# Performance work log

Hardware: AMD Instinct MI355X
Metric: run time of the kernel (lower is better)

Reference implementation:

```python
import jax, jax.numpy as jnp
import numpy as np

# FitzHugh-Nagumo / Model_FN constants (from __init__)
A_ = 0.7; B_ = 0.8; EPI = 0.2; TAU = 0.1; I_ = 1.0; K_ = 1.0; W_ = 1.0
STRENGTH = 1.0; UMAX = 10.0; D_SM = 0.1; EPS_REG = 1e-3
DIM = 1024; N = 4096


def smooth_relu(x, d=D_SM):
    r = jnp.maximum(x, 0.0)
    sq = (2.0 * d * r ** 3 - r ** 4) / (2.0 * d ** 3)
    return jnp.where(r < d, sq, x - d / 2.0)


def temp_L(t, P):
    # vectorized version of Model_FN.temp_L: sum_i eig_i * v_i^T v_i, i=1..dim-1
    dim = P.shape[0]
    i = jnp.arange(1, dim)
    s = 2.0 * K_ * jnp.sin(W_ * t)                      # [1]
    thresh = int(dim + 1) / 2 - 1                       # float threshold, as in source
    eig = jnp.where(i <= thresh, 1.0 + s, 1.0 - s)      # [dim-1]
    V = P[1:]                                           # [dim-1, dim]
    return V.T @ (eig[:, None] * V)                     # [dim, dim]


def control_net(x, W1, b1, W2, b2, W3, b3):
    # ControlNet.forward: u = MLP(x); bound(u * x)
    h1 = jnp.tanh(x @ W1.T + b1)
    h2 = jnp.tanh(h1 @ W2.T + b2)
    u = h2 @ W3.T + b3
    ux = u * x
    ux = jnp.where(ux < UMAX, ux, 0.0)
    return jnp.where(-UMAX < ux, ux, 0.0)


def icnn_fn(x, ws, bs, us):
    # ICNN.icnn_fn: x [N, d_in] -> z [1, N]
    xt = x.T                                            # [d_in, N]
    z = smooth_relu(ws[0] @ xt + bs[0])
    for i in range(len(us)):
        z = smooth_relu(ws[i + 1] @ xt + bs[i + 1] + jax.nn.softplus(us[i]) @ z)
    return z


def setup_inputs() -> dict:
    key = jax.random.key(0)
    ks = jax.random.split(key, 20)
    d_in = 2 * DIM
    inp = {
        'state': jax.random.normal(ks[0], (N, d_in), jnp.float32),
        't': jax.random.uniform(ks[1], (1,), jnp.float32) * 10.0,
        'P': jax.random.normal(ks[2], (DIM, DIM), jnp.float32) / np.sqrt(DIM),
        # ControlNet weights (SpectralNorm wrapper undefined in source -> plain Linear)
        'W1': jax.random.normal(ks[3], (512, d_in), jnp.float32) / np.sqrt(d_in),
        'b1': jax.random.normal(ks[4], (512,), jnp.float32) * 0.01,
        'W2': jax.random.normal(ks[5], (512, 512), jnp.float32) / np.sqrt(512),
        'b2': jax.random.normal(ks[6], (512,), jnp.float32) * 0.01,
        'W3': jax.random.normal(ks[7], (d_in, 512), jnp.float32) / np.sqrt(512),
        'b3': jax.random.normal(ks[8], (d_in,), jnp.float32) * 0.01,
        # ICNN parameters, layer_sizes=[64, 64, 1]
        'icW0': jax.random.normal(ks[9], (64, d_in), jnp.float32) / np.sqrt(d_in),
        'icb0': jax.random.normal(ks[10], (64, 1), jnp.float32) * 0.01,
        'icW1': jax.random.normal(ks[11], (64, d_in), jnp.float32) / np.sqrt(d_in),
        'icb1': jax.random.normal(ks[12], (64, 1), jnp.float32) * 0.01,
        'icW2': jax.random.normal(ks[13], (1, d_in), jnp.float32) / np.sqrt(d_in),
        'icb2': jax.random.normal(ks[14], (1, 1), jnp.float32) * 0.01,
        'icU0': jax.random.normal(ks[15], (64, 64), jnp.float32) / np.sqrt(64),
        'icU1': jax.random.normal(ks[16], (1, 64), jnp.float32) / np.sqrt(64),
    }
    return inp


def reference(state, t, P, W1, b1, W2, b2, W3, b3,
              icW0, icb0, icW1, icb1, icW2, icb2, icU0, icU1):
    dim = state.shape[1] // 2
    u, v = state[:, :dim], state[:, dim:]

    # FN drift with time-varying Laplacian coupling (Model_FN.FN)
    Lm = temp_L(t, P)                                   # [dim, dim]
    Hu = jax.nn.sigmoid(u / TAU)                        # H(u)
    du = u - u ** 3 / 3.0 - v + I_ + STRENGTH * (Hu @ Lm.T)
    dv = EPI * (u + A_ - B_ * v)
    dx = jnp.concatenate([du, dv], axis=1)              # [N, 2*dim]

    # ControlNet on synchronization deviations (Model_FN.FN_g state transform)
    st = jnp.concatenate([u - u[:, :1], v - v[:, :1]], axis=1)
    ctrl = control_net(st, W1, b1, W2, b2, W3, b3)
    dx_total = dx + ctrl

    # ICNN Lyapunov value (ICNN.forward)
    ws, bs, us = [icW0, icW1, icW2], [icb0, icb1, icb2], [icU0, icU1]
    z = icnn_fn(state, ws, bs, us)                      # [1, N]
    z0 = icnn_fn(jnp.zeros_like(state), ws, bs, us)     # [1, N]
    regular = EPS_REG * jnp.sum(state ** 2, axis=1, keepdims=True)
    V = smooth_relu(z - z0).T + regular                 # [N, 1]

    return jnp.concatenate([dx_total, V], axis=1)       # [N, 2*dim + 1]
```

## Files before the change

### kernel.cpp

```cpp
#include <hip/hip_runtime.h>
#include <hip/hip_fp8.h>
#include <cstdint>
#include <cstddef>

using short8 = __attribute__((ext_vector_type(8))) short;
using f32x4  = __attribute__((ext_vector_type(4))) float;
using bfraw  = unsigned short;

__device__ __forceinline__ bfraw f2b(float f){
  unsigned int u = __builtin_bit_cast(unsigned int, f);
  u += 0x7FFFu + ((u >> 16) & 1u);
  return (bfraw)(u >> 16);
}
__device__ __forceinline__ float b2f(bfraw h){
  unsigned int u = ((unsigned int)h) << 16;
  return __builtin_bit_cast(float, u);
}
__device__ __forceinline__ unsigned char f2f8(float f){
  __hip_fp8_e4m3 t(f);
  return (unsigned char)t.__x;
}
__device__ __forceinline__ float srelu(float x){
  float r = fmaxf(x, 0.0f);
  if (r < 0.1f){ float r2 = r * r; return (0.2f * r2 * r - r2 * r2) * 500.0f; }
  return x - 0.05f;
}
__device__ __forceinline__ float softplusf(float x){
  return (x > 15.0f) ? x : log1pf(expf(x));
}
__device__ __forceinline__ void gload16(const void* g, void* s){
  __builtin_amdgcn_global_load_lds((const __attribute__((address_space(1))) void*)g,
                                   (__attribute__((address_space(3))) void*)s, 16, 0, 0);
}
template<int N> __device__ __forceinline__ void wait_vm(){
  if constexpr (N == 0)      asm volatile("s_waitcnt vmcnt(0)" ::: "memory");
  else if constexpr (N == 2) asm volatile("s_waitcnt vmcnt(2)" ::: "memory");
  else if constexpr (N == 3) asm volatile("s_waitcnt vmcnt(3)" ::: "memory");
  else                       asm volatile("s_waitcnt vmcnt(4)" ::: "memory");
}
__device__ __forceinline__ void block_barrier(){
  __builtin_amdgcn_s_barrier();
  asm volatile("" ::: "memory");
}

constexpr size_t OFF_STATEB = 0;
constexpr size_t OFF_STATE8 = 16777216;
constexpr size_t OFF_HUB    = 25165824;
constexpr size_t OFF_PT     = 29360128;
constexpr size_t OFF_PTEIG  = 31457280;
constexpr size_t OFF_LM8    = 33554432;
constexpr size_t OFF_W1F8   = 34603008;
constexpr size_t OFF_ICWB   = 35651584;
constexpr size_t OFF_W28    = 36175872;
constexpr size_t OFF_W38    = 36438016;
constexpr size_t OFF_H18    = 37486592;
constexpr size_t OFF_H28    = 39583744;
constexpr size_t OFF_Z1F    = 41680896;
constexpr size_t OFF_Z2PRE  = 42729472;
constexpr size_t OFF_SPU0   = 43778048;
constexpr size_t OFF_SPU1   = 43794432;
constexpr size_t OFF_Z0     = 43794688;
constexpr size_t OFF_SU1    = 43794944;
constexpr size_t OFF_SV1    = 43796992;
constexpr size_t OFF_U0     = 43799040;
constexpr size_t OFF_V0     = 43815424;

__global__ __launch_bounds__(256) void prep_all(const float* __restrict__ W1,
    const float* __restrict__ icW0, const float* __restrict__ icW1,
    const float* __restrict__ W2, const float* __restrict__ W3,
    const float* __restrict__ P, const float* __restrict__ tptr,
    const float* __restrict__ icU0, const float* __restrict__ icU1,
    const float* __restrict__ icb0, const float* __restrict__ icb1, const float* __restrict__ icb2,
    const float* __restrict__ state,
    unsigned char* __restrict__ w1f8, bfraw* __restrict__ icwb,
    unsigned char* __restrict__ w28, unsigned char* __restrict__ w3f8,
    bfraw* __restrict__ PT, bfraw* __restrict__ PTeig,
    float* __restrict__ su1, float* __restrict__ sv1,
    float* __restrict__ spU0, float* __restrict__ spU1, float* __restrict__ z0out,
    bfraw* __restrict__ stateb, unsigned char* __restrict__ state8, unsigned char* __restrict__ hub8,
    float* __restrict__ u0a, float* __restrict__ v0a){
  __shared__ float smem[4288];
  const int b = blockIdx.x;
  const int t = threadIdx.x;
  if (b < 2560){
    const int i4 = (b * 256 + t) * 4;
    if (i4 >= 1048576 && i4 < 1310720){
      const float* src = (i4 < 1179648) ? icW0 : icW1;
      const int off = (i4 < 1179648) ? (i4 - 1048576) : (i4 - 1179648);
      const int dsto = i4 - 1048576;
      float4 v = *reinterpret_cast<const float4*>(src + off);
      ushort4 o;
      o.x = f2b(v.x); o.y = f2b(v.y); o.z = f2b(v.z); o.w = f2b(v.w);
      *reinterpret_cast<ushort4*>(icwb + dsto) = o;
    } else {
      const float* src; unsigned char* dst; int off;
      if (i4 < 1048576)      { src = W1; dst = w1f8; off = i4; }
      else if (i4 < 1572864) { src = W2; dst = w28;  off = i4 - 1310720; }
      else                   { src = W3; dst = w3f8; off = i4 - 1572864; }
      float4 v = *reinterpret_cast<const float4*>(src + off);
      uchar4 o;
      o.x = f2f8(v.x); o.y = f2f8(v.y); o.z = f2f8(v.z); o.w = f2f8(v.w);
      *reinterpret_cast<uchar4*>(dst + off) = o;
    }
  } else if (b < 3584){
    float (*tile)[33] = (float(*)[33])smem;
    const int idx = b - 2560;
    const int bi = idx >> 5, bj = idx & 31;
    const int tx = t & 31, ty = t >> 5;
    #pragma unroll
    for (int r = 0; r < 4; ++r){
      const int k = bj * 32 + ty + r * 8;
      const int i = bi * 32 + tx;
      tile[ty + r * 8][tx] = P[(size_t)k * 1024 + i];
    }
    __syncthreads();
    const float s = 2.0f * sinf(tptr[0]);
    #pragma unroll
    for (int r = 0; r < 4; ++r){
      const int i = bi * 32 + ty + r * 8;
      const int k = bj * 32 + tx;
      const float p = tile[tx][ty + r * 8];
      const float e = (k == 0) ? 0.0f : ((k <= 511) ? (1.0f + s) : (1.0f - s));
      PT[(size_t)i * 1024 + k] = f2b(p);
      PTeig[(size_t)i * 1024 + k] = f2b(e * p);
    }
  } else if (b < 4096){
    const int n = b - 3584;
    float a = 0.0f, bb = 0.0f;
    for (int j = t; j < 1024; j += 256) a += W1[(size_t)n * 2048 + j];
    for (int j = t; j < 1024; j += 256) bb += W1[(size_t)n * 2048 + 1024 + j];
    #pragma unroll
    for (int o = 32; o > 0; o >>= 1){ a += __shfl_down(a, o, 64); bb += __shfl_down(bb, o, 64); }
    if ((t & 63) == 0){ smem[t >> 6] = a; smem[4 + (t >> 6)] = bb; }
    __syncthreads();
    if (t == 0){
      su1[n] = smem[0] + smem[1] + smem[2] + smem[3];
      sv1[n] = smem[4] + smem[5] + smem[6] + smem[7];
    }
  } else if (b == 4096){
    float* sp  = smem;
    float* sp1 = smem + 4096;
    float* a0  = smem + 4160;
    float* a1  = smem + 4224;
    #pragma unroll
    for (int i = 0; i < 16; ++i){
      const int idx = i * 256 + t;
      const float v = softplusf(icU0[idx]);
      sp[idx] = v;
      spU0[idx] = v;
    }
    if (t < 64){
      const float v1 = softplusf(icU1[t]);
      sp1[t] = v1;
      spU1[t] = v1;
      a0[t] = srelu(icb0[t]);
    }
    __syncthreads();
    {
      const int n = t >> 2, q = t & 3;
      float sAcc = 0.0f;
      #pragma unroll
      for (int j = 0; j < 16; ++j) sAcc += sp[n * 64 + q * 16 + j] * a0[q * 16 + j];
      sAcc += __shfl_down(sAcc, 2, 64);
      sAcc += __shfl_down(sAcc, 1, 64);
      if (q == 0) a1[n] = srelu(sAcc + icb1[n]);
    }
    __syncthreads();
    if (t < 64){
      float v = sp1[t] * a1[t];
      #pragma unroll
      for (int o = 32; o > 0; o >>= 1) v += __shfl_down(v, o, 64);
      if (t == 0) z0out[0] = srelu(v + icb2[0]);
    }
  } else {
    const int row = b - 4097;
    const float* srow = state + (size_t)row * 2048;
    float4 u4 = *reinterpret_cast<const float4*>(srow + t * 4);
    float4 v4 = *reinterpret_cast<const float4*>(srow + 1024 + t * 4);
    float us[4] = {u4.x, u4.y, u4.z, u4.w};
    float vs[4] = {v4.x, v4.y, v4.z, v4.w};
    uchar4 h8, s8u, s8v;
    unsigned char* hp = reinterpret_cast<unsigned char*>(&h8);
    unsigned char* su = reinterpret_cast<unsigned char*>(&s8u);
    unsigned char* sv = reinterpret_cast<unsigned char*>(&s8v);
    #pragma unroll
    for (int i = 0; i < 4; ++i){
      const int j = t * 4 + i;
      const float u = us[i], v = vs[i];
      stateb[(size_t)row * 2048 + j] = f2b(u);
      stateb[(size_t)row * 2048 + 1024 + j] = f2b(v);
      su[i] = f2f8(u);
      sv[i] = f2f8(v);
      hp[i] = f2f8(1.0f / (1.0f + expf(-10.0f * u)));
    }
    *reinterpret_cast<uchar4*>(state8 + (size_t)row * 2048 + t * 4) = s8u;
    *reinterpret_cast<uchar4*>(state8 + (size_t)row * 2048 + 1024 + t * 4) = s8v;
    *reinterpret_cast<uchar4*>(hub8 + (size_t)row * 1024 + t * 4) = h8;
    if (t == 0){ u0a[row] = srow[0]; v0a[row] = srow[1024]; }
  }
}

__global__ __launch_bounds__(256) void v2_kernel(const bfraw* __restrict__ stateb, const float* __restrict__ icW2,
    const float* __restrict__ z1f, const float* __restrict__ z2pre,
    const float* __restrict__ spU0, const float* __restrict__ spU1,
    const float* __restrict__ z0p, const float* __restrict__ icb2, float* __restrict__ out){
  const int row = blockIdx.x;
  const int t = threadIdx.x;
  __shared__ float z1s[64];
  __shared__ float s1[4], s2[4];
  if (t < 64) z1s[t] = z1f[(size_t)row * 64 + t];
  short8 xv = reinterpret_cast<const short8*>(stateb + (size_t)row * 2048)[t];
  float4 w0 = reinterpret_cast<const float4*>(icW2)[t * 2];
  float4 w1 = reinterpret_cast<const float4*>(icW2)[t * 2 + 1];
  float wv[8] = {w0.x, w0.y, w0.z, w0.w, w1.x, w1.y, w1.z, w1.w};
  float d = 0.0f, ss = 0.0f;
  #pragma unroll
  for (int e = 0; e < 8; ++e){
    const float x = b2f((bfraw)xv[e]);
    d  = fmaf(wv[e], x, d);
    ss = fmaf(x, x, ss);
  }
  #pragma unroll
  for (int o = 32; o > 0; o >>= 1){ d += __shfl_down(d, o, 64); ss += __shfl_down(ss, o, 64); }
  if ((t & 63) == 0){ s1[t >> 6] = d; s2[t >> 6] = ss; }
  __syncthreads();
  if (t < 64){
    float acc2 = z2pre[(size_t)row * 64 + t];
    #pragma unroll 8
    for (int j = 0; j < 64; ++j) acc2 += spU0[t * 64 + j] * z1s[j];
    float dd = spU1[t] * srelu(acc2);
    #pragma unroll
    for (int o = 32; o > 0; o >>= 1) dd += __shfl_down(dd, o, 64);
    if (t == 0){
      const float D = dd + s1[0] + s1[1] + s1[2] + s1[3];
      const float S = s2[0] + s2[1] + s2[2] + s2[3];
      const float z3 = srelu(D + icb2[0]);
      out[(size_t)row * 2049 + 2048] = srelu(z3 - z0p[0]) + 0.001f * S;
    }
  }
}

__global__ __launch_bounds__(512)
void gemm_mid(const bfraw* __restrict__ pteig, const bfraw* __restrict__ pt,
              unsigned char* __restrict__ lm8,
              const bfraw* __restrict__ stateb, const bfraw* __restrict__ icwb,
              const float* __restrict__ icb0, const float* __restrict__ icb1,
              float* __restrict__ z1f, float* __restrict__ z2pre)
{
  __shared__ bfraw lA[3][64 * 64];
  __shared__ bfraw lB[3][64 * 64];
  const int blk = blockIdx.x;
  const bool isLm = (blk < 256);
  const bfraw* A; const bfraw* B; int K, bm, bn;
  if (isLm){ A = pteig; B = pt; K = 1024; bm = blk >> 4; bn = blk & 15; }
  else     { const int i = blk - 256; A = stateb; B = icwb; K = 2048; bm = i >> 1; bn = i & 1; }
  const int tid = threadIdx.x;
  const int w  = tid >> 6;
  const int l  = tid & 63;
  const int wr = w >> 2;
  const int wc = w & 3;
  const int lr = l & 15;
  const int q  = l >> 4;

  f32x4 acc[2] = {};
  const int nt = K >> 6;

  auto stage = [&](int buf, int k0){
    const int r = tid >> 3;
    const int kc = (tid & 7) ^ (r & 7);
    gload16(A + (size_t)(bm * 64 + r) * K + k0 + kc * 8, &lA[buf][(size_t)(w * 64) * 8]);
    gload16(B + (size_t)(bn * 64 + r) * K + k0 + kc * 8, &lB[buf][(size_t)(w * 64) * 8]);
  };

  stage(0, 0);
  stage(1, 64);
  for (int t = 0; t < nt; ++t){
    const int cur = t % 3;
    if (t == nt - 1) wait_vm<0>(); else wait_vm<2>();
    block_barrier();
    short8 aF[2][2], bF[2];
    #pragma unroll
    for (int kh = 0; kh < 2; ++kh){
      const int kch = (kh * 4 + q) ^ (lr & 7);
      #pragma unroll
      for (int m = 0; m < 2; ++m){
        const int R = wr * 32 + m * 16 + lr;
        aF[kh][m] = *reinterpret_cast<const short8*>(&lA[cur][(size_t)R * 64 + kch * 8]);
      }
      const int R = wc * 16 + lr;
      bF[kh] = *reinterpret_cast<const short8*>(&lB[cur][(size_t)R * 64 + kch * 8]);
    }
    if (t + 2 < nt) stage((t + 2) % 3, (t + 2) * 64);
    #pragma unroll
    for (int kh = 0; kh < 2; ++kh)
      #pragma unroll
      for (int m = 0; m < 2; ++m)
        acc[m] = __builtin_amdgcn_mfma_f32_16x16x32_bf16(aF[kh][m], bF[kh], acc[m], 0, 0, 0);
  }

  #pragma unroll
  for (int m = 0; m < 2; ++m){
    #pragma unroll
    for (int r = 0; r < 4; ++r){
      const int row = bm * 64 + wr * 32 + m * 16 + q * 4 + r;
      const int c64 = wc * 16 + lr;
      const float v = acc[m][r];
      if (isLm){
        lm8[(size_t)row * 1024 + bn * 64 + c64] = f2f8(v);
      } else if (bn == 0){
        z1f[(size_t)row * 64 + c64] = srelu(v + icb0[c64]);
      } else {
        z2pre[(size_t)row * 64 + c64] = v + icb1[c64];
      }
    }
  }
}

template<int EPI, int TM, int TN>
__global__ __launch_bounds__(512)
void gemm_nt8(const unsigned char* __restrict__ A, const unsigned char* __restrict__ B,
              int N, int K,
              const float* __restrict__ bias, unsigned char* __restrict__ outf8,
              const float* __restrict__ u0a, const float* __restrict__ v0a,
              const float* __restrict__ su1, const float* __restrict__ sv1)
{
  constexpr int MF = TM / 32;
  constexpr int NF = TN / 64;
  constexpr int LPB = TM / 64 + TN / 64;
  __shared__ unsigned char lA[3][TM * 128];
  __shared__ unsigned char lB[3][TN * 128];
  const int tid = threadIdx.x;
  const int w  = tid >> 6;
  const int l  = tid & 63;
  const int wr = w >> 2;
  const int wc = w & 3;
  const int bm = blockIdx.x;
  const int bn = blockIdx.y;
  const int lr = l & 15;
  const int q  = l >> 4;

  f32x4 acc[MF][NF] = {};
  const int nt = K >> 7;

  auto stage = [&](int buf, int k0){
    #pragma unroll
    for (int j = 0; j < TM / 64; ++j){
      const int c = j * 512 + tid;
      const int r = c >> 3;
      const int kc = (c & 7) ^ (r & 7);
      gload16(A + (size_t)(bm * TM + r) * K + k0 + kc * 16, &lA[buf][(size_t)(j * 512 + w * 64) * 16]);
    }
    #pragma unroll
    for (int j = 0; j < TN / 64; ++j){
      const int c = j * 512 + tid;
      const int r = c >> 3;
      const int kc = (c & 7) ^ (r & 7);
      gload16(B + (size_t)(bn * TN + r) * K + k0 + kc * 16, &lB[buf][(size_t)(j * 512 + w * 64) * 16]);
    }
  };

  stage(0, 0);
  stage(1, 128);
  for (int t = 0; t < nt; ++t){
    const int cur = t % 3;
    if (t == nt - 1) wait_vm<0>(); else wait_vm<LPB>();
    block_barrier();
    long long aF[4][MF], bF[4][NF];
    #pragma unroll
    for (int kh = 0; kh < 4; ++kh){
      const int ko = kh * 32 + q * 8;
      const int ch = (ko >> 4) ^ (lr & 7);
      const int bo = ko & 15;
      #pragma unroll
      for (int m = 0; m < MF; ++m){
        const int R = wr * (TM / 2) + m * 16 + lr;
        aF[kh][m] = *reinterpret_cast<const long long*>(&lA[cur][(size_t)R * 128 + ch * 16 + bo]);
      }
      #pragma unroll
      for (int n = 0; n < NF; ++n){
        const int R = wc * (TN / 4) + n * 16 + lr;
        bF[kh][n] = *reinterpret_cast<const long long*>(&lB[cur][(size_t)R * 128 + ch * 16 + bo]);
      }
    }
    if (t + 2 < nt) stage((t + 2) % 3, (t + 2) * 128);
    #pragma unroll
    for (int kh = 0; kh < 4; ++kh){
      #pragma unroll
      for (int m = 0; m < MF; ++m){
        #pragma unroll
        for (int n = 0; n < NF; ++n){
          acc[m][n] = __builtin_amdgcn_mfma_f32_16x16x32_fp8_fp8(aF[kh][m], bF[kh][n], acc[m][n], 0, 0, 0);
        }
      }
    }
  }

  #pragma unroll
  for (int m = 0; m < MF; ++m){
    #pragma unroll
    for (int n = 0; n < NF; ++n){
      #pragma unroll
      for (int r = 0; r < 4; ++r){
        const int row = bm * TM + wr * (TM / 2) + m * 16 + q * 4 + r;
        const int col = bn * TN + wc * (TN / 4) + n * 16 + lr;
        const float v = acc[m][n][r];
        if constexpr (EPI == 1){
          const float h = v - u0a[row] * su1[col] - v0a[row] * sv1[col] + bias[col];
          outf8[(size_t)row * N + col] = f2f8(tanhf(h));
        } else {
          outf8[(size_t)row * N + col] = f2f8(tanhf(v + bias[col]));
        }
      }
    }
  }
}

__global__ __launch_bounds__(512, 4)
void gemm_out(const unsigned char* __restrict__ hub8, const unsigned char* __restrict__ lm8,
              const unsigned char* __restrict__ h2b8, const unsigned char* __restrict__ w3f8,
              const bfraw* __restrict__ stateb, const float* __restrict__ b3,
              const float* __restrict__ u0a, const float* __restrict__ v0a,
              float* __restrict__ out)
{
  __shared__ unsigned char lA[128 * 128];
  __shared__ unsigned char lBlo[64 * 128];
  __shared__ unsigned char lBhi[64 * 128];
  const int tid = threadIdx.x;
  const int w  = tid >> 6;
  const int l  = tid & 63;
  const int wr = w >> 2;
  const int wc = w & 3;
  const int bm = blockIdx.x;
  const int bn = blockIdx.y;
  const int lr = l & 15;
  const int q  = l >> 4;

  const unsigned char* Au  = h2b8 + (size_t)(bm * 128) * 512;
  const unsigned char* Bwl = w3f8 + (size_t)(bn * 64) * 512;
  const unsigned char* Bwh = w3f8 + (size_t)(1024 + bn * 64) * 512;
  const unsigned char* Ah  = hub8 + (size_t)(bm * 128) * 1024;
  const unsigned char* Bl  = lm8  + (size_t)(bn * 64) * 1024;

  f32x4 acc2[4] = {};
  f32x4 acc3[4] = {};

  for (int t = 0; t < 4; ++t){
    const int k0 = t * 128;
    #pragma unroll
    for (int j = 0; j < 2; ++j){
      const int c = j * 512 + tid;
      const int r = c >> 3;
      const int kc = (c & 7) ^ (r & 7);
      gload16(Au + (size_t)r * 512 + k0 + kc * 16, &lA[(size_t)(j * 512 + w * 64) * 16]);
    }
    {
      const int r = tid >> 3;
      const int kc = (tid & 7) ^ (r & 7);
      gload16(Bwl + (size_t)r * 512 + k0 + kc * 16, &lBlo[(size_t)(w * 64) * 16]);
      gload16(Bwh + (size_t)r * 512 + k0 + kc * 16, &lBhi[(size_t)(w * 64) * 16]);
    }
    __syncthreads();
    #pragma unroll
    for (int kh = 0; kh < 4; ++kh){
      const int ko = kh * 32 + q * 8;
      const int ch = (ko >> 4) ^ (lr & 7);
      const int bo = ko & 15;
      long long aF[4], bL, bH;
      #pragma unroll
      for (int m = 0; m < 4; ++m){
        const int R = wr * 64 + m * 16 + lr;
        aF[m] = *reinterpret_cast<const long long*>(&lA[(size_t)R * 128 + ch * 16 + bo]);
      }
      const int Rb = wc * 16 + lr;
      bL = *reinterpret_cast<const long long*>(&lBlo[(size_t)Rb * 128 + ch * 16 + bo]);
      bH = *reinterpret_cast<const long long*>(&lBhi[(size_t)Rb * 128 + ch * 16 + bo]);
      #pragma unroll
      for (int m = 0; m < 4; ++m){
        acc2[m] = __builtin_amdgcn_mfma_f32_16x16x32_fp8_fp8(aF[m], bL, acc2[m], 0, 0, 0);
        acc3[m] = __builtin_amdgcn_mfma_f32_16x16x32_fp8_fp8(aF[m], bH, acc3[m], 0, 0, 0);
      }
    }
    __syncthreads();
  }

  #pragma unroll
  for (int m = 0; m < 4; ++m){
    #pragma unroll
    for (int r = 0; r < 4; ++r){
      const int row = bm * 128 + wr * 64 + m * 16 + q * 4 + r;
      const int c   = bn * 64 + wc * 16 + lr;
      const float un = acc3[m][r] + b3[1024 + c];
      const float u  = b2f(stateb[(size_t)row * 2048 + c]);
      const float vv = b2f(stateb[(size_t)row * 2048 + 1024 + c]);
      const float x  = vv - v0a[row];
      const float ux = un * x;
      const float cl = (ux < 10.0f && -10.0f < ux) ? ux : 0.0f;
      out[(size_t)row * 2049 + 1024 + c] = 0.2f * (u + 0.7f - 0.8f * vv) + cl;
    }
  }

  f32x4 acc1[4] = {};
  for (int t = 0; t < 8; ++t){
    const int k0 = t * 128;
    #pragma unroll
    for (int j = 0; j < 2; ++j){
      const int c = j * 512 + tid;
      const int r = c >> 3;
      const int kc = (c & 7) ^ (r & 7);
      gload16(Ah + (size_t)r * 1024 + k0 + kc * 16, &lA[(size_t)(j * 512 + w * 64) * 16]);
    }
    {
      const int r = tid >> 3;
      const int kc = (tid & 7) ^ (r & 7);
      gload16(Bl + (size_t)r * 1024 + k0 + kc * 16, &lBlo[(size_t)(w * 64) * 16]);
    }
    __syncthreads();
    #pragma unroll
    for (int kh = 0; kh < 4; ++kh){
      const int ko = kh * 32 + q * 8;
      const int ch = (ko >> 4) ^ (lr & 7);
      const int bo = ko & 15;
      long long aF[4], bL;
      #pragma unroll
      for (int m = 0; m < 4; ++m){
        const int R = wr * 64 + m * 16 + lr;
        aF[m] = *reinterpret_cast<const long long*>(&lA[(size_t)R * 128 + ch * 16 + bo]);
      }
      const int Rb = wc * 16 + lr;
      bL = *reinterpret_cast<const long long*>(&lBlo[(size_t)Rb * 128 + ch * 16 + bo]);
      #pragma unroll
      for (int m = 0; m < 4; ++m){
        acc1[m] = __builtin_amdgcn_mfma_f32_16x16x32_fp8_fp8(aF[m], bL, acc1[m], 0, 0, 0);
      }
    }
    __syncthreads();
  }

  #pragma unroll
  for (int m = 0; m < 4; ++m){
    #pragma unroll
    for (int r = 0; r < 4; ++r){
      const int row = bm * 128 + wr * 64 + m * 16 + q * 4 + r;
      const int c   = bn * 64 + wc * 16 + lr;
      const float un = acc2[m][r] + b3[c];
      const float u  = b2f(stateb[(size_t)row * 2048 + c]);
      const float vv = b2f(stateb[(size_t)row * 2048 + 1024 + c]);
      const float x  = u - u0a[row];
      const float ux = un * x;
      const float cl = (ux < 10.0f && -10.0f < ux) ? ux : 0.0f;
      out[(size_t)row * 2049 + c] = acc1[m][r] + u - u * u * u * (1.0f / 3.0f) - vv + 1.0f + cl;
    }
  }
}

extern "C" void kernel_launch(void* const* d_in, const int* in_sizes, int n_in,
                              void* d_out, int out_size, void* d_ws, size_t ws_size,
                              hipStream_t stream){
  (void)in_sizes; (void)n_in; (void)out_size; (void)ws_size;
  const float* state = (const float*)d_in[0];
  const float* tp    = (const float*)d_in[1];
  const float* P     = (const float*)d_in[2];
  const float* W1    = (const float*)d_in[3];
  const float* b1    = (const float*)d_in[4];
  const float* W2    = (const float*)d_in[5];
  const float* b2    = (const float*)d_in[6];
  const float* W3    = (const float*)d_in[7];
  const float* b3    = (const float*)d_in[8];
  const float* icW0  = (const float*)d_in[9];
  const float* icb0  = (const float*)d_in[10];
  const float* icW1  = (const float*)d_in[11];
  const float* icb1  = (const float*)d_in[12];
  const float* icW2  = (const float*)d_in[13];
  const float* icb2  = (const float*)d_in[14];
  const float* icU0  = (const float*)d_in[15];
  const float* icU1  = (const float*)d_in[16];
  float* out = (float*)d_out;
  char* ws = (char*)d_ws;

  bfraw* stateb = (bfraw*)(ws + OFF_STATEB);
  unsigned char* state8 = (unsigned char*)(ws + OFF_STATE8);
  unsigned char* hub8   = (unsigned char*)(ws + OFF_HUB);
  bfraw* pt     = (bfraw*)(ws + OFF_PT);
  bfraw* pteig  = (bfraw*)(ws + OFF_PTEIG);
  unsigned char* lm8  = (unsigned char*)(ws + OFF_LM8);
  unsigned char* w1f8 = (unsigned char*)(ws + OFF_W1F8);
  bfraw* icwb   = (bfraw*)(ws + OFF_ICWB);
  unsigned char* w28  = (unsigned char*)(ws + OFF_W28);
  unsigned char* w3f8 = (unsigned char*)(ws + OFF_W38);
  unsigned char* h18  = (unsigned char*)(ws + OFF_H18);
  unsigned char* h28  = (unsigned char*)(ws + OFF_H28);
  float* z1f    = (float*)(ws + OFF_Z1F);
  float* z2pre  = (float*)(ws + OFF_Z2PRE);
  float* spU0   = (float*)(ws + OFF_SPU0);
  float* spU1   = (float*)(ws + OFF_SPU1);
  float* z0     = (float*)(ws + OFF_Z0);
  float* su1    = (float*)(ws + OFF_SU1);
  float* sv1    = (float*)(ws + OFF_SV1);
  float* u0a    = (float*)(ws + OFF_U0);
  float* v0a    = (float*)(ws + OFF_V0);

  prep_all<<<dim3(8193), 256, 0, stream>>>(W1, icW0, icW1, W2, W3, P, tp,
      icU0, icU1, icb0, icb1, icb2, state,
      w1f8, icwb, w28, w3f8, pt, pteig, su1, sv1, spU0, spU1, z0,
      stateb, state8, hub8, u0a, v0a);

  gemm_mid<<<dim3(384), 512, 0, stream>>>(pteig, pt, lm8, stateb, icwb, icb0, icb1, z1f, z2pre);
  gemm_nt8<1, 64, 128><<<dim3(64, 4), 512, 0, stream>>>(state8, w1f8, 512, 2048,
      b1, h18, u0a, v0a, su1, sv1);
  gemm_nt8<2, 64, 128><<<dim3(64, 4), 512, 0, stream>>>(h18, w28, 512, 512,
      b2, h28, nullptr, nullptr, nullptr, nullptr);
  gemm_out<<<dim3(32, 16), 512, 0, stream>>>(hub8, lm8, h28, w3f8, stateb, b3, u0a, v0a, out);

  v2_kernel<<<dim3(4096), 256, 0, stream>>>(stateb, icW2, z1f, z2pre, spU0, spU1, z0, icb2, out);
}
```

Before: 101.5 us.

## Merge independent kernels via block-index dispatch to cut launch count

Folds the first ControlNet layer GEMM into the Laplacian/ICNN mid GEMM launch as extra blocks, and folds the per-row ICNN value kernel into the output GEMM launch as trailing blocks using a shared raw LDS buffer. This takes the pipeline from six launches to four and lets independent work share one grid, reducing launch gaps and tail idle time. The value blocks now use 512 threads with 4 elements each. The costs are larger LDS allocations for the merged blocks, which can lower occupancy, and mixed block types inside one grid.

New measurement: 95.37 us, median of 2. 1.06x faster.

```diff
diff --git a/kernel.cpp b/kernel.cpp
--- a/kernel.cpp
+++ b/kernel.cpp
@@ -200,135 +200,164 @@
   }
 }
 
-__global__ __launch_bounds__(256) void v2_kernel(const bfraw* __restrict__ stateb, const float* __restrict__ icW2,
-    const float* __restrict__ z1f, const float* __restrict__ z2pre,
-    const float* __restrict__ spU0, const float* __restrict__ spU1,
-    const float* __restrict__ z0p, const float* __restrict__ icb2, float* __restrict__ out){
-  const int row = blockIdx.x;
-  const int t = threadIdx.x;
-  __shared__ float z1s[64];
-  __shared__ float s1[4], s2[4];
-  if (t < 64) z1s[t] = z1f[(size_t)row * 64 + t];
-  short8 xv = reinterpret_cast<const short8*>(stateb + (size_t)row * 2048)[t];
-  float4 w0 = reinterpret_cast<const float4*>(icW2)[t * 2];
-  float4 w1 = reinterpret_cast<const float4*>(icW2)[t * 2 + 1];
-  float wv[8] = {w0.x, w0.y, w0.z, w0.w, w1.x, w1.y, w1.z, w1.w};
-  float d = 0.0f, ss = 0.0f;
-  #pragma unroll
-  for (int e = 0; e < 8; ++e){
-    const float x = b2f((bfraw)xv[e]);
-    d  = fmaf(wv[e], x, d);
-    ss = fmaf(x, x, ss);
-  }
-  #pragma unroll
-  for (int o = 32; o > 0; o >>= 1){ d += __shfl_down(d, o, 64); ss += __shfl_down(ss, o, 64); }
-  if ((t & 63) == 0){ s1[t >> 6] = d; s2[t >> 6] = ss; }
-  __syncthreads();
-  if (t < 64){
-    float acc2 = z2pre[(size_t)row * 64 + t];
-    #pragma unroll 8
-    for (int j = 0; j < 64; ++j) acc2 += spU0[t * 64 + j] * z1s[j];
-    float dd = spU1[t] * srelu(acc2);
-    #pragma unroll
-    for (int o = 32; o > 0; o >>= 1) dd += __shfl_down(dd, o, 64);
-    if (t == 0){
-      const float D = dd + s1[0] + s1[1] + s1[2] + s1[3];
-      const float S = s2[0] + s2[1] + s2[2] + s2[3];
-      const float z3 = srelu(D + icb2[0]);
-      out[(size_t)row * 2049 + 2048] = srelu(z3 - z0p[0]) + 0.001f * S;
-    }
-  }
-}
-
 __global__ __launch_bounds__(512)
-void gemm_mid(const bfraw* __restrict__ pteig, const bfraw* __restrict__ pt,
-              unsigned char* __restrict__ lm8,
-              const bfraw* __restrict__ stateb, const bfraw* __restrict__ icwb,
-              const float* __restrict__ icb0, const float* __restrict__ icb1,
-              float* __restrict__ z1f, float* __restrict__ z2pre)
+void gemm_midh1(const bfraw* __restrict__ pteig, const bfraw* __restrict__ pt,
+                unsigned char* __restrict__ lm8,
+                const bfraw* __restrict__ stateb, const bfraw* __restrict__ icwb,
+                const float* __restrict__ icb0, const float* __restrict__ icb1,
+                float* __restrict__ z1f, float* __restrict__ z2pre,
+                const unsigned char* __restrict__ state8, const unsigned char* __restrict__ w1f8,
+                const float* __restrict__ b1, unsigned char* __restrict__ h18,
+                const float* __restrict__ u0a, const float* __restrict__ v0a,
+                const float* __restrict__ su1, const float* __restrict__ sv1)
 {
-  __shared__ bfraw lA[3][64 * 64];
-  __shared__ bfraw lB[3][64 * 64];
+  __shared__ char ldsRaw[73728];
   const int blk = blockIdx.x;
-  const bool isLm = (blk < 256);
-  const bfraw* A; const bfraw* B; int K, bm, bn;
-  if (isLm){ A = pteig; B = pt; K = 1024; bm = blk >> 4; bn = blk & 15; }
-  else     { const int i = blk - 256; A = stateb; B = icwb; K = 2048; bm = i >> 1; bn = i & 1; }
   const int tid = threadIdx.x;
   const int w  = tid >> 6;
   const int l  = tid & 63;
-  const int wr = w >> 2;
-  const int wc = w & 3;
   const int lr = l & 15;
   const int q  = l >> 4;
 
-  f32x4 acc[2] = {};
-  const int nt = K >> 6;
-
-  auto stage = [&](int buf, int k0){
-    const int r = tid >> 3;
-    const int kc = (tid & 7) ^ (r & 7);
-    gload16(A + (size_t)(bm * 64 + r) * K + k0 + kc * 8, &lA[buf][(size_t)(w * 64) * 8]);
-    gload16(B + (size_t)(bn * 64 + r) * K + k0 + kc * 8, &lB[buf][(size_t)(w * 64) * 8]);
-  };
-
-  stage(0, 0);
-  stage(1, 64);
-  for (int t = 0; t < nt; ++t){
-    const int cur = t % 3;
-    if (t == nt - 1) wait_vm<0>(); else wait_vm<2>();
-    block_barrier();
-    short8 aF[2][2], bF[2];
-    #pragma unroll
-    for (int kh = 0; kh < 2; ++kh){
-      const int kch = (kh * 4 + q) ^ (lr & 7);
-      #pragma unroll
-      for (int m = 0; m < 2; ++m){
-        const int R = wr * 32 + m * 16 + lr;
-        aF[kh][m] = *reinterpret_cast<const short8*>(&lA[cur][(size_t)R * 64 + kch * 8]);
-      }
-      const int R = wc * 16 + lr;
-      bF[kh] = *reinterpret_cast<const short8*>(&lB[cur][(size_t)R * 64 + kch * 8]);
-    }
-    if (t + 2 < nt) stage((t + 2) % 3, (t + 2) * 64);
-    #pragma unroll
-    for (int kh = 0; kh < 2; ++kh)
-      #pragma unroll
-      for (int m = 0; m < 2; ++m)
-        acc[m] = __builtin_amdgcn_mfma_f32_16x16x32_bf16(aF[kh][m], bF[kh], acc[m], 0, 0, 0);
-  }
-
-  #pragma unroll
-  for (int m = 0; m < 2; ++m){
-    #pragma unroll
-    for (int r = 0; r < 4; ++r){
-      const int row = bm * 64 + wr * 32 + m * 16 + q * 4 + r;
-      const int c64 = wc * 16 + lr;
-      const float v = acc[m][r];
-      if (isLm){
-        lm8[(size_t)row * 1024 + bn * 64 + c64] = f2f8(v);
-      } else if (bn == 0){
-        z1f[(size_t)row * 64 + c64] = srelu(v + icb0[c64]);
-      } else {
-        z2pre[(size_t)row * 64 + c64] = v + icb1[c64];
-      }
-    }
-  }
-}
-
-template<int EPI, int TM, int TN>
+  if (blk < 384){
+    bfraw* lA = (bfraw*)ldsRaw;
+    bfraw* lB = (bfraw*)(ldsRaw + 24576);
+    const bool isLm = (blk < 256);
+    const bfraw* A; const bfraw* B; int K, bm, bn;
+    if (isLm){ A = pteig; B = pt; K = 1024; bm = blk >> 4; bn = blk & 15; }
+    else     { const int i = blk - 256; A = stateb; B = icwb; K = 2048; bm = i >> 1; bn = i & 1; }
+    const int wr = w >> 2;
+    const int wc = w & 3;
+    f32x4 acc[2] = {};
+    const int nt = K >> 6;
+    auto stage = [&](int buf, int k0){
+      const int r = tid >> 3;
+      const int kc = (tid & 7) ^ (r & 7);
+      gload16(A + (size_t)(bm * 64 + r) * K + k0 + kc * 8, &lA[(size_t)buf * 4096 + (size_t)(w * 64) * 8]);
+      gload16(B + (size_t)(bn * 64 + r) * K + k0 + kc * 8, &lB[(size_t)buf * 4096 + (size_t)(w * 64) * 8]);
+    };
+    stage(0, 0);
+    stage(1, 64);
+    for (int t = 0; t < nt; ++t){
+      const int cur = t % 3;
+      if (t == nt - 1) wait_vm<0>(); else wait_vm<2>();
+      block_barrier();
+      short8 aF[2][2], bF[2];
+      #pragma unroll
+      for (int kh = 0; kh < 2; ++kh){
+        const int kch = (kh * 4 + q) ^ (lr & 7);
+        #pragma unroll
+        for (int m = 0; m < 2; ++m){
+          const int R = wr * 32 + m * 16 + lr;
+          aF[kh][m] = *reinterpret_cast<const short8*>(&lA[(size_t)cur * 4096 + (size_t)R * 64 + kch * 8]);
+        }
+        const int R = wc * 16 + lr;
+        bF[kh] = *reinterpret_cast<const short8*>(&lB[(size_t)cur * 4096 + (size_t)R * 64 + kch * 8]);
+      }
+      if (t + 2 < nt) stage((t + 2) % 3, (t + 2) * 64);
+      #pragma unroll
+      for (int kh = 0; kh < 2; ++kh)
+        #pragma unroll
+        for (int m = 0; m < 2; ++m)
+          acc[m] = __builtin_amdgcn_mfma_f32_16x16x32_bf16(aF[kh][m], bF[kh], acc[m], 0, 0, 0);
+    }
+    #pragma unroll
+    for (int m = 0; m < 2; ++m){
+      #pragma unroll
+      for (int r = 0; r < 4; ++r){
+        const int row = bm * 64 + (w >> 2) * 32 + m * 16 + q * 4 + r;
+        const int c64 = (w & 3) * 16 + lr;
+        const float v = acc[m][r];
+        if (isLm){
+          lm8[(size_t)row * 1024 + bn * 64 + c64] = f2f8(v);
+        } else if (bn == 0){
+          z1f[(size_t)row * 64 + c64] = srelu(v + icb0[c64]);
+        } else {
+          z2pre[(size_t)row * 64 + c64] = v + icb1[c64];
+        }
+      }
+    }
+  } else {
+    unsigned char* lA = (unsigned char*)ldsRaw;
+    unsigned char* lB = (unsigned char*)(ldsRaw + 24576);
+    const int i = blk - 384;
+    const int bm = i >> 2;
+    const int bn = i & 3;
+    const int wr = w >> 2;
+    const int wc = w & 3;
+    constexpr int K = 2048;
+    f32x4 acc[2][2] = {};
+    const int nt = K >> 7;
+    auto stage = [&](int buf, int k0){
+      {
+        const int c = tid;
+        const int r = c >> 3;
+        const int kc = (c & 7) ^ (r & 7);
+        gload16(state8 + (size_t)(bm * 64 + r) * K + k0 + kc * 16, &lA[(size_t)buf * 8192 + (size_t)(w * 64) * 16]);
+      }
+      #pragma unroll
+      for (int j = 0; j < 2; ++j){
+        const int c = j * 512 + tid;
+        const int r = c >> 3;
+        const int kc = (c & 7) ^ (r & 7);
+        gload16(w1f8 + (size_t)(bn * 128 + r) * K + k0 + kc * 16, &lB[(size_t)buf * 16384 + (size_t)(j * 512 + w * 64) * 16]);
+      }
+    };
+    stage(0, 0);
+    stage(1, 128);
+    for (int t = 0; t < nt; ++t){
+      const int cur = t % 3;
+      if (t == nt - 1) wait_vm<0>(); else wait_vm<3>();
+      block_barrier();
+      long long aF[4][2], bF[4][2];
+      #pragma unroll
+      for (int kh = 0; kh < 4; ++kh){
+        const int ko = kh * 32 + q * 8;
+        const int ch = (ko >> 4) ^ (lr & 7);
+        const int bo = ko & 15;
+        #pragma unroll
+        for (int m = 0; m < 2; ++m){
+          const int R = wr * 32 + m * 16 + lr;
+          aF[kh][m] = *reinterpret_cast<const long long*>(&lA[(size_t)cur * 8192 + (size_t)R * 128 + ch * 16 + bo]);
+        }
+        #pragma unroll
+        for (int n = 0; n < 2; ++n){
+          const int R = wc * 32 + n * 16 + lr;
+          bF[kh][n] = *reinterpret_cast<const long long*>(&lB[(size_t)cur * 16384 + (size_t)R * 128 + ch * 16 + bo]);
+        }
+      }
+      if (t + 2 < nt) stage((t + 2) % 3, (t + 2) * 128);
+      #pragma unroll
+      for (int kh = 0; kh < 4; ++kh)
+        #pragma unroll
+        for (int m = 0; m < 2; ++m)
+          #pragma unroll
+          for (int n = 0; n < 2; ++n)
+            acc[m][n] = __builtin_amdgcn_mfma_f32_16x16x32_fp8_fp8(aF[kh][m], bF[kh][n], acc[m][n], 0, 0, 0);
+    }
+    #pragma unroll
+    for (int m = 0; m < 2; ++m){
+      #pragma unroll
+      for (int n = 0; n < 2; ++n){
+        #pragma unroll
+        for (int r = 0; r < 4; ++r){
+          const int row = bm * 64 + wr * 32 + m * 16 + q * 4 + r;
+          const int col = bn * 128 + wc * 32 + n * 16 + lr;
+          const float h = acc[m][n][r] - u0a[row] * su1[col] - v0a[row] * sv1[col] + b1[col];
+          h18[(size_t)row * 512 + col] = f2f8(tanhf(h));
+        }
+      }
+    }
+  }
+}
+
 __global__ __launch_bounds__(512)
-void gemm_nt8(const unsigned char* __restrict__ A, const unsigned char* __restrict__ B,
-              int N, int K,
-              const float* __restrict__ bias, unsigned char* __restrict__ outf8,
-              const float* __restrict__ u0a, const float* __restrict__ v0a,
-              const float* __restrict__ su1, const float* __restrict__ sv1)
+void gemm_h2(const unsigned char* __restrict__ A, const unsigned char* __restrict__ B,
+             const float* __restrict__ bias, unsigned char* __restrict__ outf8)
 {
-  constexpr int MF = TM / 32;
-  constexpr int NF = TN / 64;
-  constexpr int LPB = TM / 64 + TN / 64;
-  __shared__ unsigned char lA[3][TM * 128];
-  __shared__ unsigned char lB[3][TN * 128];
+  constexpr int N = 512, K = 512;
+  __shared__ unsigned char lA[3][64 * 128];
+  __shared__ unsigned char lB[3][128 * 128];
   const int tid = threadIdx.x;
   const int w  = tid >> 6;
   const int l  = tid & 63;
@@ -338,100 +367,132 @@
   const int bn = blockIdx.y;
   const int lr = l & 15;
   const int q  = l >> 4;
-
-  f32x4 acc[MF][NF] = {};
+  f32x4 acc[2][2] = {};
   const int nt = K >> 7;
-
   auto stage = [&](int buf, int k0){
-    #pragma unroll
-    for (int j = 0; j < TM / 64; ++j){
+    {
+      const int c = tid;
+      const int r = c >> 3;
+      const int kc = (c & 7) ^ (r & 7);
+      gload16(A + (size_t)(bm * 64 + r) * K + k0 + kc * 16, &lA[buf][(size_t)(w * 64) * 16]);
+    }
+    #pragma unroll
+    for (int j = 0; j < 2; ++j){
       const int c = j * 512 + tid;
       const int r = c >> 3;
       const int kc = (c & 7) ^ (r & 7);
-      gload16(A + (size_t)(bm * TM + r) * K + k0 + kc * 16, &lA[buf][(size_t)(j * 512 + w * 64) * 16]);
-    }
-    #pragma unroll
-    for (int j = 0; j < TN / 64; ++j){
-      const int c = j * 512 + tid;
-      const int r = c >> 3;
-      const int kc = (c & 7) ^ (r & 7);
-      gload16(B + (size_t)(bn * TN + r) * K + k0 + kc * 16, &lB[buf][(size_t)(j * 512 + w * 64) * 16]);
+      gload16(B + (size_t)(bn * 128 + r) * K + k0 + kc * 16, &lB[buf][(size_t)(j * 512 + w * 64) * 16]);
     }
   };
-
   stage(0, 0);
   stage(1, 128);
   for (int t = 0; t < nt; ++t){
     const int cur = t % 3;
-    if (t == nt - 1) wait_vm<0>(); else wait_vm<LPB>();
+    if (t == nt - 1) wait_vm<0>(); else wait_vm<3>();
     block_barrier();
-    long long aF[4][MF], bF[4][NF];
+    long long aF[4][2], bF[4][2];
     #pragma unroll
     for (int kh = 0; kh < 4; ++kh){
       const int ko = kh * 32 + q * 8;
       const int ch = (ko >> 4) ^ (lr & 7);
       const int bo = ko & 15;
       #pragma unroll
-      for (int m = 0; m < MF; ++m){
-        const int R = wr * (TM / 2) + m * 16 + lr;
+      for (int m = 0; m < 2; ++m){
+        const int R = wr * 32 + m * 16 + lr;
         aF[kh][m] = *reinterpret_cast<const long long*>(&lA[cur][(size_t)R * 128 + ch * 16 + bo]);
       }
       #pragma unroll
-      for (int n = 0; n < NF; ++n){
-        const int R = wc * (TN / 4) + n * 16 + lr;
+      for (int n = 0; n < 2; ++n){
+        const int R = wc * 32 + n * 16 + lr;
         bF[kh][n] = *reinterpret_cast<const long long*>(&lB[cur][(size_t)R * 128 + ch * 16 + bo]);
       }
     }
     if (t + 2 < nt) stage((t + 2) % 3, (t + 2) * 128);
     #pragma unroll
-    for (int kh = 0; kh < 4; ++kh){
-      #pragma unroll
-      for (int m = 0; m < MF; ++m){
-        #pragma unroll
-        for (int n = 0; n < NF; ++n){
+    for (int kh = 0; kh < 4; ++kh)
+      #pragma unroll
+      for (int m = 0; m < 2; ++m)
+        #pragma unroll
+        for (int n = 0; n < 2; ++n)
           acc[m][n] = __builtin_amdgcn_mfma_f32_16x16x32_fp8_fp8(aF[kh][m], bF[kh][n], acc[m][n], 0, 0, 0);
-        }
-      }
-    }
-  }
-
+  }
   #pragma unroll
-  for (int m = 0; m < MF; ++m){
-    #pragma unroll
-    for (int n = 0; n < NF; ++n){
+  for (int m = 0; m < 2; ++m){
+    #pragma unroll
+    for (int n = 0; n < 2; ++n){
       #pragma unroll
       for (int r = 0; r < 4; ++r){
-        const int row = bm * TM + wr * (TM / 2) + m * 16 + q * 4 + r;
-        const int col = bn * TN + wc * (TN / 4) + n * 16 + lr;
-        const float v = acc[m][n][r];
-        if constexpr (EPI == 1){
-          const float h = v - u0a[row] * su1[col] - v0a[row] * sv1[col] + bias[col];
-          outf8[(size_t)row * N + col] = f2f8(tanhf(h));
-        } else {
-          outf8[(size_t)row * N + col] = f2f8(tanhf(v + bias[col]));
-        }
+        const int row = bm * 64 + wr * 32 + m * 16 + q * 4 + r;
+        const int col = bn * 128 + wc * 32 + n * 16 + lr;
+        outf8[(size_t)row * N + col] = f2f8(tanhf(acc[m][n][r] + bias[col]));
       }
     }
   }
 }
 
 __global__ __launch_bounds__(512, 4)
-void gemm_out(const unsigned char* __restrict__ hub8, const unsigned char* __restrict__ lm8,
-              const unsigned char* __restrict__ h2b8, const unsigned char* __restrict__ w3f8,
-              const bfraw* __restrict__ stateb, const float* __restrict__ b3,
-              const float* __restrict__ u0a, const float* __restrict__ v0a,
-              float* __restrict__ out)
+void gemm_outv2(const unsigned char* __restrict__ hub8, const unsigned char* __restrict__ lm8,
+                const unsigned char* __restrict__ h2b8, const unsigned char* __restrict__ w3f8,
+                const bfraw* __restrict__ stateb, const float* __restrict__ b3,
+                const float* __restrict__ u0a, const float* __restrict__ v0a,
+                const float* __restrict__ icW2, const float* __restrict__ z1f,
+                const float* __restrict__ z2pre, const float* __restrict__ spU0,
+                const float* __restrict__ spU1, const float* __restrict__ z0p,
+                const float* __restrict__ icb2,
+                float* __restrict__ out)
 {
-  __shared__ unsigned char lA[128 * 128];
-  __shared__ unsigned char lBlo[64 * 128];
-  __shared__ unsigned char lBhi[64 * 128];
+  __shared__ char ldsRaw[32768 + 512];
+  const int blk = blockIdx.x;
   const int tid = threadIdx.x;
+
+  if (blk >= 512){
+    float* z1s = (float*)ldsRaw;
+    float* s1  = (float*)(ldsRaw + 256);
+    float* s2  = (float*)(ldsRaw + 288);
+    const int row = blk - 512;
+    if (tid < 64) z1s[tid] = z1f[(size_t)row * 64 + tid];
+    ushort4 xv = reinterpret_cast<const ushort4*>(stateb + (size_t)row * 2048)[tid];
+    float4 wv = reinterpret_cast<const float4*>(icW2)[tid];
+    bfraw xr[4] = {xv.x, xv.y, xv.z, xv.w};
+    float wr4[4] = {wv.x, wv.y, wv.z, wv.w};
+    float d = 0.0f, ss = 0.0f;
+    #pragma unroll
+    for (int e = 0; e < 4; ++e){
+      const float x = b2f(xr[e]);
+      d  = fmaf(wr4[e], x, d);
+      ss = fmaf(x, x, ss);
+    }
+    #pragma unroll
+    for (int o = 32; o > 0; o >>= 1){ d += __shfl_down(d, o, 64); ss += __shfl_down(ss, o, 64); }
+    if ((tid & 63) == 0){ s1[tid >> 6] = d; s2[tid >> 6] = ss; }
+    __syncthreads();
+    if (tid < 64){
+      float acc2 = z2pre[(size_t)row * 64 + tid];
+      #pragma unroll 8
+      for (int j = 0; j < 64; ++j) acc2 += spU0[tid * 64 + j] * z1s[j];
+      float dd = spU1[tid] * srelu(acc2);
+      #pragma unroll
+      for (int o = 32; o > 0; o >>= 1) dd += __shfl_down(dd, o, 64);
+      if (tid == 0){
+        float D = dd, S = 0.0f;
+        #pragma unroll
+        for (int k = 0; k < 8; ++k){ D += s1[k]; S += s2[k]; }
+        const float z3 = srelu(D + icb2[0]);
+        out[(size_t)row * 2049 + 2048] = srelu(z3 - z0p[0]) + 0.001f * S;
+      }
+    }
+    return;
+  }
+
+  unsigned char* lA   = (unsigned char*)ldsRaw;
+  unsigned char* lBlo = (unsigned char*)(ldsRaw + 16384);
+  unsigned char* lBhi = (unsigned char*)(ldsRaw + 24576);
   const int w  = tid >> 6;
   const int l  = tid & 63;
   const int wr = w >> 2;
   const int wc = w & 3;
-  const int bm = blockIdx.x;
-  const int bn = blockIdx.y;
+  const int bm = blk & 31;
+  const int bn = blk >> 5;
   const int lr = l & 15;
   const int q  = l >> 4;
 
@@ -604,12 +665,9 @@
       w1f8, icwb, w28, w3f8, pt, pteig, su1, sv1, spU0, spU1, z0,
       stateb, state8, hub8, u0a, v0a);
 
-  gemm_mid<<<dim3(384), 512, 0, stream>>>(pteig, pt, lm8, stateb, icwb, icb0, icb1, z1f, z2pre);
-  gemm_nt8<1, 64, 128><<<dim3(64, 4), 512, 0, stream>>>(state8, w1f8, 512, 2048,
-      b1, h18, u0a, v0a, su1, sv1);
-  gemm_nt8<2, 64, 128><<<dim3(64, 4), 512, 0, stream>>>(h18, w28, 512, 512,
-      b2, h28, nullptr, nullptr, nullptr, nullptr);
-  gemm_out<<<dim3(32, 16), 512, 0, stream>>>(hub8, lm8, h28, w3f8, stateb, b3, u0a, v0a, out);
-
-  v2_kernel<<<dim3(4096), 256, 0, stream>>>(stateb, icW2, z1f, z2pre, spU0, spU1, z0, icb2, out);
-}
+  gemm_midh1<<<dim3(640), 512, 0, stream>>>(pteig, pt, lm8, stateb, icwb, icb0, icb1,
+      z1f, z2pre, state8, w1f8, b1, h18, u0a, v0a, su1, sv1);
+  gemm_h2<<<dim3(64, 4), 512, 0, stream>>>(h18, w28, b2, h28);
+  gemm_outv2<<<dim3(4608), 512, 0, stream>>>(hub8, lm8, h28, w3f8, stateb, b3, u0a, v0a,
+      icW2, z1f, z2pre, spU0, spU1, z0, icb2, out);
+}
```
